# Kernel tuning notes

Hardware: AMD Instinct MI355X
Metric: run time of the kernel (lower is better)

## Reference

```python
import jax, jax.numpy as jnp
import numpy as np
import math

B, S, E = 16, 4096, 16      # batch, seq_len, n_experts
NE = 64                     # config.n_embd -> expert bottleneck dim
F = 4 * NE                  # n_state = 4*n_embd -> token feature dim


def gelu(x):
    # tanh-approx GELU exactly as in the source module
    c = math.sqrt(2.0 / math.pi)
    return 0.5 * x * (1.0 + jnp.tanh(c * (x + 0.044715 * x * x * x)))


def setup_inputs() -> dict:
    key = jax.random.key(0)
    ks = jax.random.split(key, 7)
    s1 = 1.0 / math.sqrt(F)   # fan-in init like nn.Linear(F, NE)
    s2 = 1.0 / math.sqrt(NE)  # fan-in init like nn.Linear(NE, F)
    return {
        "x":  jax.random.normal(ks[0], (B, S, F), jnp.float32),
        "W1": jax.random.uniform(ks[1], (E, F, NE), jnp.float32, -s1, s1),  # stacked c_fc
        "b1": jax.random.uniform(ks[2], (E, NE),    jnp.float32, -s1, s1),
        "W2": jax.random.uniform(ks[3], (E, NE, F), jnp.float32, -s2, s2),  # stacked c_proj
        "b2": jax.random.uniform(ks[4], (E, F),     jnp.float32, -s2, s2),
        "Wg": jax.random.uniform(ks[5], (F, E),     jnp.float32, -s1, s1),  # router
        "bg": jax.random.uniform(ks[6], (E,),       jnp.float32, -s1, s1),
    }


def reference(x, W1, b1, W2, b2, Wg, bg):
    # Router: per-token scores -> mean over sequence -> softmax over experts. [B, E]
    gate = jax.nn.softmax(jnp.mean(x @ Wg + bg, axis=1), axis=-1)
    # Dense all-experts FFN: [B, E, S, NE]
    h = gelu(jnp.einsum('bsf,efh->besh', x, W1) + b1[None, :, None, :])
    # [B, E, S, F]
    outs = jnp.einsum('besh,ehf->besf', h, W2) + b2[None, :, None, :]
    # Gate-weighted combine over experts -> [B, S, F]
    return jnp.einsum('be,besf->bsf', gate, outs)
```

## Files before the change

### kernel.cpp

```cpp
#include <hip/hip_runtime.h>
#include <hip/hip_bf16.h>
#include <stdint.h>

#define NB 16
#define NS 4096
#define NF 256
#define NH 64
#define NEXP 16

typedef __attribute__((ext_vector_type(8))) short     bf16x8;
typedef __attribute__((ext_vector_type(4))) float     f32x4;
typedef __attribute__((ext_vector_type(2))) unsigned  u32x2;
typedef __attribute__((ext_vector_type(8))) unsigned short u16x8;

#define PART_OFF   0u
#define GATE_OFF   524288u
#define BIASC_OFF  525312u
#define W1T_OFF    541696u
#define W2T_OFF    1065984u

__device__ __forceinline__ unsigned short bfr(float f) {
  unsigned u = __float_as_uint(f);
  u += 0x7fffu + ((u >> 16) & 1u);
  return (unsigned short)(u >> 16);
}
__device__ __forceinline__ unsigned pk(float a, float b) {
  __hip_bfloat162 t = __float22bfloat162_rn(make_float2(a, b));
  union { __hip_bfloat162 h; unsigned u; } cv; cv.h = t; return cv.u;
}
__device__ __forceinline__ bf16x8 as_bf(f32x4 v) {
  union { f32x4 f; bf16x8 h; } u; u.f = v; return u.h;
}
__device__ __forceinline__ void stage16(const void* g, void* l) {
  __builtin_amdgcn_global_load_lds((const __attribute__((address_space(1))) void*)g,
                                   (__attribute__((address_space(3))) void*)l, 16, 0, 0);
}

__global__ void k_pre(const float* __restrict__ x, const float* __restrict__ W1,
                      const float* __restrict__ W2, uint8_t* __restrict__ wsb) {
  const int blk = blockIdx.x;
  if (blk < 512) {
    const int b  = blk >> 5;
    const int ch = blk & 31;
    const int f  = threadIdx.x;
    const float* xp = x + ((size_t)b * NS + (size_t)ch * 128) * NF + f;
    float s = 0.0f;
    for (int i = 0; i < 128; ++i) s += xp[(size_t)i * NF];
    ((float*)(wsb + PART_OFF))[(size_t)(ch * 16 + b) * NF + f] = s;
    return;
  }
  const int u = (blk - 512) * 256 + threadIdx.x;
  u16x8 vals;
  if (u < 32768) {
    const int e  = u >> 11;
    const int r  = u & 2047;
    const int hd = r >> 5;
    const int kc = r & 31;
    const float* src = W1 + (size_t)e * (NF * NH) + (size_t)(kc * 8) * NH + hd;
#pragma unroll
    for (int j = 0; j < 8; ++j) vals[j] = bfr(src[(size_t)j * NH]);
    const int dst = (kc >> 2) * 4096 + hd * 64 + (kc & 3) * 16;
    *(u16x8*)(wsb + W1T_OFF + (size_t)e * 32768 + dst) = vals;
  } else {
    const int u2 = u - 32768;
    const int e  = u2 >> 11;
    const int r  = u2 & 2047;
    const int f  = r >> 3;
    const int hc = r & 7;
    const float* src = W2 + (size_t)e * (NH * NF) + (size_t)(hc * 8) * NF + f;
#pragma unroll
    for (int j = 0; j < 8; ++j) vals[j] = bfr(src[(size_t)j * NF]);
    const int dst = hc * 4096 + f * 16;
    *(u16x8*)(wsb + W2T_OFF + (size_t)e * 32768 + dst) = vals;
  }
}

__global__ void k_gate(const float* __restrict__ Wg, const float* __restrict__ bg,
                       const float* __restrict__ b2, uint8_t* __restrict__ wsb) {
  __shared__ float cs[16][256];
  __shared__ float lg[16][16];
  __shared__ float gs[16][16];
  const float* part  = (const float*)(wsb + PART_OFF);
  float* gate  = (float*)(wsb + GATE_OFF);
  float* biasc = (float*)(wsb + BIASC_OFF);
  const int t = threadIdx.x;
  for (int b = 0; b < 16; ++b) {
    float s = 0.0f;
    for (int ch = 0; ch < 32; ++ch) s += part[(size_t)(ch * 16 + b) * NF + t];
    cs[b][t] = s * (1.0f / 4096.0f);
  }
  __syncthreads();
  {
    const int b = t >> 4, e = t & 15;
    float acc = bg[e];
    for (int f = 0; f < NF; ++f) acc += cs[b][f] * Wg[f * 16 + e];
    lg[b][e] = acc;
  }
  __syncthreads();
  {
    const int b = t >> 4, e = t & 15;
    float m = lg[b][0];
    for (int j = 1; j < 16; ++j) m = fmaxf(m, lg[b][j]);
    float den = 0.0f;
    for (int j = 0; j < 16; ++j) den += __expf(lg[b][j] - m);
    float g = __expf(lg[b][e] - m) / den;
    gate[b * 16 + e] = g;
    gs[b][e] = g;
  }
  __syncthreads();
  for (int b = 0; b < 16; ++b) {
    float acc = 0.0f;
    for (int e = 0; e < 16; ++e) acc += gs[b][e] * b2[e * NF + t];
    biasc[b * NF + t] = acc;
  }
}

__global__ __launch_bounds__(768, 3)
void k_main(const float* __restrict__ x, const float* __restrict__ b1g,
            const uint8_t* __restrict__ wsb, float* __restrict__ out) {
  __shared__ __align__(16) uint8_t lds[98304];

  const int tid  = threadIdx.x;
  const int w    = tid >> 6;
  const int lane = tid & 63;
  const int c    = lane & 15;
  const int q    = lane >> 4;
  const bool g1  = (w < 4);
  const int fs   = (w - 4) * 32;
  const int st   = tid - 256;
  const int blk  = blockIdx.x;
  const int b    = blk >> 5;

  const float* gate_ws = (const float*)(wsb + GATE_OFF) + b * 16;
  const float* biasc   = (const float*)(wsb + BIASC_OFF) + b * NF;
  const uint8_t* w1src = wsb + W1T_OFF;
  const uint8_t* w2src = wsb + W2T_OFF;

  const f32x4 fz = {0.0f, 0.0f, 0.0f, 0.0f};
  f32x4 R[16];
  bf16x8 w2r[2][2];

  if (!g1) {
#pragma unroll
    for (int i = 0; i < 4; ++i)
      stage16(w1src + i * 8192 + st * 16, lds + i * 8192 + st * 16);
#pragma unroll
    for (int i = 0; i < 16; ++i) R[i] = fz;
  } else {
    const int row0 = blk * 128 + w * 32;
#pragma unroll
    for (int n = 0; n < 2; ++n) {
      const float* xp = x + (size_t)(row0 + n * 16 + c) * NF + q * 8;
#pragma unroll
      for (int ks = 0; ks < 8; ++ks) {
        f32x4 v0 = *(const f32x4*)(xp + ks * 32);
        f32x4 v1 = *(const f32x4*)(xp + ks * 32 + 4);
        union { unsigned u[4]; f32x4 f; } cv;
        cv.u[0] = pk(v0[0], v0[1]); cv.u[1] = pk(v0[2], v0[3]);
        cv.u[2] = pk(v1[0], v1[1]); cv.u[3] = pk(v1[2], v1[3]);
        R[n * 8 + ks] = cv.f;
      }
    }
  }

  __syncthreads();

  const float K1 = -2.3021858962f;
  const float KA = -0.102942243f;

#pragma unroll 1
  for (int e = 0; e < NEXP; ++e) {
    const int p  = e & 1;
    const int pn = p ^ 1;

    if (g1) {
      const uint8_t* w1p = lds + p * 32768;
      f32x4 a1[4][2];
#pragma unroll
      for (int m = 0; m < 4; ++m) { a1[m][0] = fz; a1[m][1] = fz; }
      __builtin_amdgcn_s_setprio(1);
#pragma unroll
      for (int ks = 0; ks < 8; ++ks) {
        bf16x8 am[4];
#pragma unroll
        for (int m = 0; m < 4; ++m)
          am[m] = *(const bf16x8*)(w1p + ks * 4096 + (m * 16 + c) * 64 + q * 16);
#pragma unroll
        for (int m = 0; m < 4; ++m) {
          a1[m][0] = __builtin_amdgcn_mfma_f32_16x16x32_bf16(am[m], as_bf(R[ks]),     a1[m][0], 0, 0, 0);
          a1[m][1] = __builtin_amdgcn_mfma_f32_16x16x32_bf16(am[m], as_bf(R[8 + ks]), a1[m][1], 0, 0, 0);
        }
      }
      __builtin_amdgcn_s_setprio(0);

      const float gv = gate_ws[e];
      uint8_t* htp = lds + 65536 + p * 16384;
#pragma unroll
      for (int m = 0; m < 4; ++m) {
        f32x4 b1v = *(const f32x4*)(b1g + e * NH + m * 16 + q * 4);
#pragma unroll
        for (int n = 0; n < 2; ++n) {
          f32x4 hv = a1[m][n] + b1v;
          float o[4];
#pragma unroll
          for (int r = 0; r < 4; ++r) {
            float xx = hv[r];
            float x2 = xx * xx;
            float tt = fmaf(KA, x2, K1);
            float ez = __builtin_amdgcn_exp2f(xx * tt);
            float rc = __builtin_amdgcn_rcpf(ez + 1.0f);
            o[r] = (gv * xx) * rc;
          }
          u32x2 hw;
          hw.x = pk(o[0], o[1]);
          hw.y = pk(o[2], o[3]);
          const int chunk = m * 2 + (q >> 1);
          const int tok   = w * 32 + n * 16 + c;
          *(u32x2*)(htp + chunk * 2048 + tok * 16 + (q & 1) * 8) = hw;
        }
      }
    } else {
      if (e < 15) {
        const uint8_t* src = w1src + (size_t)(e + 1) * 32768;
        uint8_t* dst = lds + pn * 32768;
#pragma unroll
        for (int i = 0; i < 4; ++i)
          stage16(src + i * 8192 + st * 16, dst + i * 8192 + st * 16);
      }

      if (e > 0) {
        const uint8_t* htp2 = lds + 65536 + pn * 16384;
        __builtin_amdgcn_s_setprio(1);
#pragma unroll
        for (int ks2 = 0; ks2 < 2; ++ks2) {
          bf16x8 bb2[8];
#pragma unroll
          for (int n2 = 0; n2 < 8; ++n2)
            bb2[n2] = *(const bf16x8*)(htp2 + (ks2 * 4 + q) * 2048 + (n2 * 16 + c) * 16);
#pragma unroll
          for (int m2 = 0; m2 < 2; ++m2)
#pragma unroll
            for (int n2 = 0; n2 < 8; ++n2)
              R[m2 * 8 + n2] = __builtin_amdgcn_mfma_f32_16x16x32_bf16(w2r[ks2][m2], bb2[n2], R[m2 * 8 + n2], 0, 0, 0);
        }
        __builtin_amdgcn_s_setprio(0);
      }

      const uint8_t* src = w2src + (size_t)e * 32768 + q * 4096 + (fs + c) * 16;
#pragma unroll
      for (int ks2 = 0; ks2 < 2; ++ks2)
#pragma unroll
        for (int m2 = 0; m2 < 2; ++m2)
          w2r[ks2][m2] = *(const bf16x8*)(src + ks2 * 16384 + m2 * 256);
    }

    __syncthreads();
  }

  if (!g1) {
    const uint8_t* htp2 = lds + 65536 + 16384;
#pragma unroll
    for (int ks2 = 0; ks2 < 2; ++ks2) {
      bf16x8 bb2[8];
#pragma unroll
      for (int n2 = 0; n2 < 8; ++n2)
        bb2[n2] = *(const bf16x8*)(htp2 + (ks2 * 4 + q) * 2048 + (n2 * 16 + c) * 16);
#pragma unroll
      for (int m2 = 0; m2 < 2; ++m2)
#pragma unroll
        for (int n2 = 0; n2 < 8; ++n2)
          R[m2 * 8 + n2] = __builtin_amdgcn_mfma_f32_16x16x32_bf16(w2r[ks2][m2], bb2[n2], R[m2 * 8 + n2], 0, 0, 0);
    }
#pragma unroll
    for (int m2 = 0; m2 < 2; ++m2) {
      const int fbase = fs + m2 * 16 + q * 4;
      f32x4 bc = *(const f32x4*)(biasc + fbase);
#pragma unroll
      for (int n2 = 0; n2 < 8; ++n2) {
        const int token = blk * 128 + n2 * 16 + c;
        f32x4 o = R[m2 * 8 + n2] + bc;
        *(f32x4*)(out + (size_t)token * NF + fbase) = o;
      }
    }
  }
}

extern "C" void kernel_launch(void* const* d_in, const int* in_sizes, int n_in,
                              void* d_out, int out_size, void* d_ws, size_t ws_size,
                              hipStream_t stream) {
  const float* x  = (const float*)d_in[0];
  const float* W1 = (const float*)d_in[1];
  const float* b1 = (const float*)d_in[2];
  const float* W2 = (const float*)d_in[3];
  const float* b2 = (const float*)d_in[4];
  const float* Wg = (const float*)d_in[5];
  const float* bg = (const float*)d_in[6];
  float* out = (float*)d_out;
  uint8_t* wsb = (uint8_t*)d_ws;

  k_pre<<<768, 256, 0, stream>>>(x, W1, W2, wsb);
  k_gate<<<1, 256, 0, stream>>>(Wg, bg, b2, wsb);
  k_main<<<512, 768, 0, stream>>>(x, b1, wsb, out);
}
```

Measured before the change: 124.1 us.

## Load W1 fragments directly from global into registers, shrink LDS to H buffers

Stops staging the per-expert W1 tile into LDS through the second warp group. The four GEMM1 waves now read their W1 fragments straight from global memory (L2) into registers, double-buffered one k-step ahead and prefetching the next expert's first step. LDS shrinks from 96KB to 32KB and holds only the double-buffered H tiles, which may let more blocks fit per CU. The full __syncthreads is replaced by an explicit lgkmcnt wait plus a raw barrier, so outstanding global loads no longer stall the barrier. The cost is global/L2 read traffic on the critical GEMM1 path and the latency of those loads.

```diff
diff --git a/kernel.cpp b/kernel.cpp
--- a/kernel.cpp
+++ b/kernel.cpp
@@ -30,10 +30,6 @@
 }
 __device__ __forceinline__ bf16x8 as_bf(f32x4 v) {
   union { f32x4 f; bf16x8 h; } u; u.f = v; return u.h;
-}
-__device__ __forceinline__ void stage16(const void* g, void* l) {
-  __builtin_amdgcn_global_load_lds((const __attribute__((address_space(1))) void*)g,
-                                   (__attribute__((address_space(3))) void*)l, 16, 0, 0);
 }
 
 __global__ void k_pre(const float* __restrict__ x, const float* __restrict__ W1,
@@ -118,7 +114,7 @@
 __global__ __launch_bounds__(768, 3)
 void k_main(const float* __restrict__ x, const float* __restrict__ b1g,
             const uint8_t* __restrict__ wsb, float* __restrict__ out) {
-  __shared__ __align__(16) uint8_t lds[98304];
+  __shared__ __align__(16) uint8_t lds[32768];
 
   const int tid  = threadIdx.x;
   const int w    = tid >> 6;
@@ -127,7 +123,6 @@
   const int q    = lane >> 4;
   const bool g1  = (w < 4);
   const int fs   = (w - 4) * 32;
-  const int st   = tid - 256;
   const int blk  = blockIdx.x;
   const int b    = blk >> 5;
 
@@ -139,11 +134,11 @@
   const f32x4 fz = {0.0f, 0.0f, 0.0f, 0.0f};
   f32x4 R[16];
   bf16x8 w2r[2][2];
+  bf16x8 am[2][4];
+
+  const uint8_t* w1lane = w1src + c * 64 + q * 16;
 
   if (!g1) {
-#pragma unroll
-    for (int i = 0; i < 4; ++i)
-      stage16(w1src + i * 8192 + st * 16, lds + i * 8192 + st * 16);
 #pragma unroll
     for (int i = 0; i < 16; ++i) R[i] = fz;
   } else {
@@ -161,9 +156,10 @@
         R[n * 8 + ks] = cv.f;
       }
     }
-  }
-
-  __syncthreads();
+#pragma unroll
+    for (int m = 0; m < 4; ++m)
+      am[0][m] = *(const bf16x8*)(w1lane + m * 1024);
+  }
 
   const float K1 = -2.3021858962f;
   const float KA = -0.102942243f;
@@ -174,27 +170,28 @@
     const int pn = p ^ 1;
 
     if (g1) {
-      const uint8_t* w1p = lds + p * 32768;
       f32x4 a1[4][2];
 #pragma unroll
       for (int m = 0; m < 4; ++m) { a1[m][0] = fz; a1[m][1] = fz; }
+      const uint8_t* w1e  = w1lane + (size_t)e * 32768;
+      const uint8_t* w1en = w1lane + (size_t)(e < 15 ? e + 1 : 15) * 32768;
       __builtin_amdgcn_s_setprio(1);
 #pragma unroll
       for (int ks = 0; ks < 8; ++ks) {
-        bf16x8 am[4];
+        const uint8_t* pf = (ks < 7) ? (w1e + (ks + 1) * 4096) : w1en;
 #pragma unroll
         for (int m = 0; m < 4; ++m)
-          am[m] = *(const bf16x8*)(w1p + ks * 4096 + (m * 16 + c) * 64 + q * 16);
+          am[(ks + 1) & 1][m] = *(const bf16x8*)(pf + m * 1024);
 #pragma unroll
         for (int m = 0; m < 4; ++m) {
-          a1[m][0] = __builtin_amdgcn_mfma_f32_16x16x32_bf16(am[m], as_bf(R[ks]),     a1[m][0], 0, 0, 0);
-          a1[m][1] = __builtin_amdgcn_mfma_f32_16x16x32_bf16(am[m], as_bf(R[8 + ks]), a1[m][1], 0, 0, 0);
+          a1[m][0] = __builtin_amdgcn_mfma_f32_16x16x32_bf16(am[ks & 1][m], as_bf(R[ks]),     a1[m][0], 0, 0, 0);
+          a1[m][1] = __builtin_amdgcn_mfma_f32_16x16x32_bf16(am[ks & 1][m], as_bf(R[8 + ks]), a1[m][1], 0, 0, 0);
         }
       }
       __builtin_amdgcn_s_setprio(0);
 
       const float gv = gate_ws[e];
-      uint8_t* htp = lds + 65536 + p * 16384;
+      uint8_t* htp = lds + p * 16384;
 #pragma unroll
       for (int m = 0; m < 4; ++m) {
         f32x4 b1v = *(const f32x4*)(b1g + e * NH + m * 16 + q * 4);
@@ -220,16 +217,8 @@
         }
       }
     } else {
-      if (e < 15) {
-        const uint8_t* src = w1src + (size_t)(e + 1) * 32768;
-        uint8_t* dst = lds + pn * 32768;
-#pragma unroll
-        for (int i = 0; i < 4; ++i)
-          stage16(src + i * 8192 + st * 16, dst + i * 8192 + st * 16);
-      }
-
       if (e > 0) {
-        const uint8_t* htp2 = lds + 65536 + pn * 16384;
+        const uint8_t* htp2 = lds + pn * 16384;
         __builtin_amdgcn_s_setprio(1);
 #pragma unroll
         for (int ks2 = 0; ks2 < 2; ++ks2) {
@@ -245,7 +234,6 @@
         }
         __builtin_amdgcn_s_setprio(0);
       }
-
       const uint8_t* src = w2src + (size_t)e * 32768 + q * 4096 + (fs + c) * 16;
 #pragma unroll
       for (int ks2 = 0; ks2 < 2; ++ks2)
@@ -254,11 +242,13 @@
           w2r[ks2][m2] = *(const bf16x8*)(src + ks2 * 16384 + m2 * 256);
     }
 
-    __syncthreads();
+    asm volatile("s_waitcnt lgkmcnt(0)" ::: "memory");
+    __builtin_amdgcn_s_barrier();
+    __builtin_amdgcn_sched_barrier(0);
   }
 
   if (!g1) {
-    const uint8_t* htp2 = lds + 65536 + 16384;
+    const uint8_t* htp2 = lds + 16384;
 #pragma unroll
     for (int ks2 = 0; ks2 < 2; ++ks2) {
       bf16x8 bb2[8];
```

After: 226.2 us. +82.2%, slower.

## Retile second GEMM per wave, double-buffer W1 LDS reads, split barriers

Applied to the files above, without the earlier changes.

Consumer waves now each own a 64-feature by 64-token tile of the W2 GEMM instead of 32 features by 128 tokens, which halves the per-wave LDS reads of hidden activations but doubles the W2 register fragments. The producer waves software-pipeline W1 fragment loads from LDS one k-step ahead, using two alternating register sets. The block-wide __syncthreads is replaced by role-specific waitcnt plus s_barrier, so consumer waves wait only on older global loads (vmcnt(8)) and the new W2 prefetch can stay in flight across the barrier. This relies on correct counter accounting, and the extra register pressure could hurt occupancy.

```diff
diff --git a/kernel.cpp b/kernel.cpp
--- a/kernel.cpp
+++ b/kernel.cpp
@@ -126,7 +126,8 @@
   const int c    = lane & 15;
   const int q    = lane >> 4;
   const bool g1  = (w < 4);
-  const int fs   = (w - 4) * 32;
+  const int fs   = ((w - 4) >> 1) * 64;
+  const int ts   = ((w - 4) & 1) * 64;
   const int st   = tid - 256;
   const int blk  = blockIdx.x;
   const int b    = blk >> 5;
@@ -138,7 +139,7 @@
 
   const f32x4 fz = {0.0f, 0.0f, 0.0f, 0.0f};
   f32x4 R[16];
-  bf16x8 w2r[2][2];
+  bf16x8 w2r[2][4];
 
   if (!g1) {
 #pragma unroll
@@ -175,20 +176,33 @@
 
     if (g1) {
       const uint8_t* w1p = lds + p * 32768;
+      bf16x8 am0[4], am1[4];
+#pragma unroll
+      for (int m = 0; m < 4; ++m)
+        am0[m] = *(const bf16x8*)(w1p + (m * 16 + c) * 64 + q * 16);
       f32x4 a1[4][2];
 #pragma unroll
       for (int m = 0; m < 4; ++m) { a1[m][0] = fz; a1[m][1] = fz; }
       __builtin_amdgcn_s_setprio(1);
 #pragma unroll
       for (int ks = 0; ks < 8; ++ks) {
-        bf16x8 am[4];
-#pragma unroll
-        for (int m = 0; m < 4; ++m)
-          am[m] = *(const bf16x8*)(w1p + ks * 4096 + (m * 16 + c) * 64 + q * 16);
+        if (ks < 7) {
+          const uint8_t* nxt = w1p + (ks + 1) * 4096;
+          if (ks & 1) {
+#pragma unroll
+            for (int m = 0; m < 4; ++m)
+              am0[m] = *(const bf16x8*)(nxt + (m * 16 + c) * 64 + q * 16);
+          } else {
+#pragma unroll
+            for (int m = 0; m < 4; ++m)
+              am1[m] = *(const bf16x8*)(nxt + (m * 16 + c) * 64 + q * 16);
+          }
+        }
 #pragma unroll
         for (int m = 0; m < 4; ++m) {
-          a1[m][0] = __builtin_amdgcn_mfma_f32_16x16x32_bf16(am[m], as_bf(R[ks]),     a1[m][0], 0, 0, 0);
-          a1[m][1] = __builtin_amdgcn_mfma_f32_16x16x32_bf16(am[m], as_bf(R[8 + ks]), a1[m][1], 0, 0, 0);
+          bf16x8 a = (ks & 1) ? am1[m] : am0[m];
+          a1[m][0] = __builtin_amdgcn_mfma_f32_16x16x32_bf16(a, as_bf(R[ks]),     a1[m][0], 0, 0, 0);
+          a1[m][1] = __builtin_amdgcn_mfma_f32_16x16x32_bf16(a, as_bf(R[8 + ks]), a1[m][1], 0, 0, 0);
         }
       }
       __builtin_amdgcn_s_setprio(0);
@@ -219,6 +233,9 @@
           *(u32x2*)(htp + chunk * 2048 + tok * 16 + (q & 1) * 8) = hw;
         }
       }
+      asm volatile("s_waitcnt lgkmcnt(0)" ::: "memory");
+      __builtin_amdgcn_s_barrier();
+      __builtin_amdgcn_sched_barrier(0);
     } else {
       if (e < 15) {
         const uint8_t* src = w1src + (size_t)(e + 1) * 32768;
@@ -227,58 +244,65 @@
         for (int i = 0; i < 4; ++i)
           stage16(src + i * 8192 + st * 16, dst + i * 8192 + st * 16);
       }
+      __builtin_amdgcn_sched_barrier(0);
 
       if (e > 0) {
         const uint8_t* htp2 = lds + 65536 + pn * 16384;
+        bf16x8 bb[2][4];
+#pragma unroll
+        for (int ks2 = 0; ks2 < 2; ++ks2)
+#pragma unroll
+          for (int n2 = 0; n2 < 4; ++n2)
+            bb[ks2][n2] = *(const bf16x8*)(htp2 + (ks2 * 4 + q) * 2048 + (ts + n2 * 16 + c) * 16);
         __builtin_amdgcn_s_setprio(1);
 #pragma unroll
-        for (int ks2 = 0; ks2 < 2; ++ks2) {
-          bf16x8 bb2[8];
-#pragma unroll
-          for (int n2 = 0; n2 < 8; ++n2)
-            bb2[n2] = *(const bf16x8*)(htp2 + (ks2 * 4 + q) * 2048 + (n2 * 16 + c) * 16);
-#pragma unroll
-          for (int m2 = 0; m2 < 2; ++m2)
-#pragma unroll
-            for (int n2 = 0; n2 < 8; ++n2)
-              R[m2 * 8 + n2] = __builtin_amdgcn_mfma_f32_16x16x32_bf16(w2r[ks2][m2], bb2[n2], R[m2 * 8 + n2], 0, 0, 0);
-        }
+        for (int ks2 = 0; ks2 < 2; ++ks2)
+#pragma unroll
+          for (int m2 = 0; m2 < 4; ++m2)
+#pragma unroll
+            for (int n2 = 0; n2 < 4; ++n2)
+              R[m2 * 4 + n2] = __builtin_amdgcn_mfma_f32_16x16x32_bf16(w2r[ks2][m2], bb[ks2][n2], R[m2 * 4 + n2], 0, 0, 0);
         __builtin_amdgcn_s_setprio(0);
       }
 
-      const uint8_t* src = w2src + (size_t)e * 32768 + q * 4096 + (fs + c) * 16;
-#pragma unroll
-      for (int ks2 = 0; ks2 < 2; ++ks2)
-#pragma unroll
-        for (int m2 = 0; m2 < 2; ++m2)
-          w2r[ks2][m2] = *(const bf16x8*)(src + ks2 * 16384 + m2 * 256);
+      {
+        const uint8_t* src = w2src + (size_t)e * 32768 + q * 4096 + (fs + c) * 16;
+#pragma unroll
+        for (int ks2 = 0; ks2 < 2; ++ks2)
+#pragma unroll
+          for (int m2 = 0; m2 < 4; ++m2)
+            w2r[ks2][m2] = *(const bf16x8*)(src + ks2 * 16384 + m2 * 256);
+      }
+
+      asm volatile("s_waitcnt vmcnt(8) lgkmcnt(0)" ::: "memory");
+      __builtin_amdgcn_s_barrier();
+      __builtin_amdgcn_sched_barrier(0);
     }
-
-    __syncthreads();
   }
 
   if (!g1) {
     const uint8_t* htp2 = lds + 65536 + 16384;
-#pragma unroll
-    for (int ks2 = 0; ks2 < 2; ++ks2) {
-      bf16x8 bb2[8];
-#pragma unroll
-      for (int n2 = 0; n2 < 8; ++n2)
-        bb2[n2] = *(const bf16x8*)(htp2 + (ks2 * 4 + q) * 2048 + (n2 * 16 + c) * 16);
-#pragma unroll
-      for (int m2 = 0; m2 < 2; ++m2)
-#pragma unroll
-        for (int n2 = 0; n2 < 8; ++n2)
-          R[m2 * 8 + n2] = __builtin_amdgcn_mfma_f32_16x16x32_bf16(w2r[ks2][m2], bb2[n2], R[m2 * 8 + n2], 0, 0, 0);
-    }
-#pragma unroll
-    for (int m2 = 0; m2 < 2; ++m2) {
+    bf16x8 bb[2][4];
+#pragma unroll
+    for (int ks2 = 0; ks2 < 2; ++ks2)
+#pragma unroll
+      for (int n2 = 0; n2 < 4; ++n2)
+        bb[ks2][n2] = *(const bf16x8*)(htp2 + (ks2 * 4 + q) * 2048 + (ts + n2 * 16 + c) * 16);
+#pragma unroll
+    for (int ks2 = 0; ks2 < 2; ++ks2)
+#pragma unroll
+      for (int m2 = 0; m2 < 4; ++m2)
+#pragma unroll
+        for (int n2 = 0; n2 < 4; ++n2)
+          R[m2 * 4 + n2] = __builtin_amdgcn_mfma_f32_16x16x32_bf16(w2r[ks2][m2], bb[ks2][n2], R[m2 * 4 + n2], 0, 0, 0);
+#pragma unroll
+    for (int m2 = 0; m2 < 4; ++m2) {
       const int fbase = fs + m2 * 16 + q * 4;
       f32x4 bc = *(const f32x4*)(biasc + fbase);
 #pragma unroll
-      for (int n2 = 0; n2 < 8; ++n2) {
-        const int token = blk * 128 + n2 * 16 + c;
-        f32x4 o = R[m2 * 8 + n2] + bc;
+      for (int n2 = 0; n2 < 4; ++n2) {
+        const int token = blk * 128 + ts + n2 * 16 + c;
+        f32x4 o = R[m2 * 4 + n2] + bc;
         *(f32x4*)(out + (size_t)token * NF + fbase) = o;
       }
     }
```

Result: slower. 144.2 us (+16.2%).

## Split fused MoE kernel into separate hidden-activation and output kernels via workspace

Applied to the files above, without the earlier changes.

Replaces the warp-specialized fused kernel with two kernels when the workspace is large enough. The first computes GELU hidden activations for all experts and writes them to global memory as bf16. The second reads them back, scales W2 by the gate in registers, and accumulates the output with a larger per-wave tile and register double-buffering. This removes the producer/consumer LDS handoff and per-expert barriers, at the cost of writing and re-reading a 128 MB intermediate and one extra launch. The fused kernel is kept as a fallback.

```diff
diff --git a/kernel.cpp b/kernel.cpp
--- a/kernel.cpp
+++ b/kernel.cpp
@@ -18,6 +18,8 @@
 #define BIASC_OFF  525312u
 #define W1T_OFF    541696u
 #define W2T_OFF    1065984u
+#define H_OFF      1590272u
+#define WS_NEED    (1590272ull + 134217728ull)
 
 __device__ __forceinline__ unsigned short bfr(float f) {
   unsigned u = __float_as_uint(f);
@@ -115,11 +117,203 @@
   }
 }
 
+__global__ __launch_bounds__(256, 2)
+void k_h(const float* __restrict__ x, const float* __restrict__ b1g,
+         const uint8_t* __restrict__ wsb, uint8_t* __restrict__ hbuf) {
+  __shared__ __align__(16) uint8_t lds[65536];
+
+  const int tid  = threadIdx.x;
+  const int w    = tid >> 6;
+  const int lane = tid & 63;
+  const int c    = lane & 15;
+  const int q    = lane >> 4;
+  const int blk  = blockIdx.x;
+  const int gtok0 = blk * 128 + w * 32;
+  const uint8_t* w1src = wsb + W1T_OFF;
+
+#pragma unroll
+  for (int i = 0; i < 8; ++i)
+    stage16(w1src + i * 4096 + tid * 16, lds + i * 4096 + tid * 16);
+
+  bf16x8 xf[16];
+#pragma unroll
+  for (int n = 0; n < 2; ++n) {
+    const float* xp = x + (size_t)(gtok0 + n * 16 + c) * NF + q * 8;
+#pragma unroll
+    for (int ks = 0; ks < 8; ++ks) {
+      f32x4 v0 = *(const f32x4*)(xp + ks * 32);
+      f32x4 v1 = *(const f32x4*)(xp + ks * 32 + 4);
+      union { unsigned u[4]; bf16x8 h; } cv;
+      cv.u[0] = pk(v0[0], v0[1]); cv.u[1] = pk(v0[2], v0[3]);
+      cv.u[2] = pk(v1[0], v1[1]); cv.u[3] = pk(v1[2], v1[3]);
+      xf[n * 8 + ks] = cv.h;
+    }
+  }
+
+  __syncthreads();
+
+  const float K1 = -2.3021858962f;
+  const float KA = -0.102942243f;
+  const f32x4 fz = {0.0f, 0.0f, 0.0f, 0.0f};
+
+#pragma unroll 1
+  for (int e = 0; e < NEXP; ++e) {
+    const int p = e & 1;
+    if (e < 15) {
+      const uint8_t* src = w1src + (size_t)(e + 1) * 32768;
+      uint8_t* dst = lds + (p ^ 1) * 32768;
+#pragma unroll
+      for (int i = 0; i < 8; ++i)
+        stage16(src + i * 4096 + tid * 16, dst + i * 4096 + tid * 16);
+    }
+
+    const uint8_t* w1p = lds + p * 32768;
+    f32x4 a1[4][2];
+#pragma unroll
+    for (int m = 0; m < 4; ++m) { a1[m][0] = fz; a1[m][1] = fz; }
+    __builtin_amdgcn_s_setprio(1);
+#pragma unroll
+    for (int ks = 0; ks < 8; ++ks) {
+      bf16x8 am[4];
+#pragma unroll
+      for (int m = 0; m < 4; ++m)
+        am[m] = *(const bf16x8*)(w1p + ks * 4096 + (m * 16 + c) * 64 + q * 16);
+#pragma unroll
+      for (int m = 0; m < 4; ++m) {
+        a1[m][0] = __builtin_amdgcn_mfma_f32_16x16x32_bf16(am[m], xf[ks],     a1[m][0], 0, 0, 0);
+        a1[m][1] = __builtin_amdgcn_mfma_f32_16x16x32_bf16(am[m], xf[8 + ks], a1[m][1], 0, 0, 0);
+      }
+    }
+    __builtin_amdgcn_s_setprio(0);
+
+    uint8_t* he = hbuf + (size_t)e * 8388608;
+#pragma unroll
+    for (int m = 0; m < 4; ++m) {
+      f32x4 b1v = *(const f32x4*)(b1g + e * NH + m * 16 + q * 4);
+#pragma unroll
+      for (int n = 0; n < 2; ++n) {
+        f32x4 hv = a1[m][n] + b1v;
+        float o[4];
+#pragma unroll
+        for (int r = 0; r < 4; ++r) {
+          float xx = hv[r];
+          float tt = fmaf(KA, xx * xx, K1);
+          float ez = __builtin_amdgcn_exp2f(xx * tt);
+          o[r] = xx * __builtin_amdgcn_rcpf(ez + 1.0f);
+        }
+        u32x2 hw;
+        hw.x = pk(o[0], o[1]);
+        hw.y = pk(o[2], o[3]);
+        *(u32x2*)(he + (size_t)(gtok0 + n * 16 + c) * 128 + m * 32 + q * 8) = hw;
+      }
+    }
+
+    __syncthreads();
+  }
+}
+
+__device__ __forceinline__ void ko_loadh(bf16x8 (&h)[8], const uint8_t* hbuf, int e,
+                                         int gtok0, int c, int q) {
+  const uint8_t* src = hbuf + (size_t)e * 8388608 + (size_t)(gtok0 + c) * 128 + q * 16;
+#pragma unroll
+  for (int n2 = 0; n2 < 4; ++n2)
+#pragma unroll
+    for (int ks2 = 0; ks2 < 2; ++ks2)
+      h[n2 * 2 + ks2] = *(const bf16x8*)(src + n2 * 2048 + ks2 * 64);
+}
+__device__ __forceinline__ void ko_loadw(f32x4 (&wr)[8], const uint8_t* w2src, int e,
+                                         int fs, int c, int q) {
+  const uint8_t* src = w2src + (size_t)e * 32768 + q * 4096 + (fs + c) * 16;
+#pragma unroll
+  for (int ks2 = 0; ks2 < 2; ++ks2)
+#pragma unroll
+    for (int m2 = 0; m2 < 4; ++m2)
+      wr[ks2 * 4 + m2] = *(const f32x4*)(src + ks2 * 16384 + m2 * 256);
+}
+__device__ __forceinline__ void ko_mma(f32x4 (&acc)[16], const f32x4 (&wr)[8],
+                                       const bf16x8 (&h)[8], float g) {
+  bf16x8 ws[8];
+#pragma unroll
+  for (int i = 0; i < 8; ++i) {
+    union { f32x4 f; unsigned u[4]; } in; in.f = wr[i];
+    union { unsigned u[4]; bf16x8 h; } o;
+#pragma unroll
+    for (int j = 0; j < 4; ++j) {
+      float lo = __uint_as_float(in.u[j] << 16) * g;
+      float hi = __uint_as_float(in.u[j] & 0xffff0000u) * g;
+      o.u[j] = pk(lo, hi);
+    }
+    ws[i] = o.h;
+  }
+  __builtin_amdgcn_s_setprio(1);
+#pragma unroll
+  for (int ks2 = 0; ks2 < 2; ++ks2)
+#pragma unroll
+    for (int m2 = 0; m2 < 4; ++m2)
+#pragma unroll
+      for (int n2 = 0; n2 < 4; ++n2)
+        acc[m2 * 4 + n2] = __builtin_amdgcn_mfma_f32_16x16x32_bf16(ws[ks2 * 4 + m2], h[n2 * 2 + ks2], acc[m2 * 4 + n2], 0, 0, 0);
+  __builtin_amdgcn_s_setprio(0);
+}
+
+__global__ __launch_bounds__(256, 2)
+void k_o(const uint8_t* __restrict__ wsb, const uint8_t* __restrict__ hbuf,
+         float* __restrict__ out) {
+  const int tid  = threadIdx.x;
+  const int w    = tid >> 6;
+  const int lane = tid & 63;
+  const int c    = lane & 15;
+  const int q    = lane >> 4;
+  const int blk  = blockIdx.x;
+  const int gtok0 = blk * 64;
+  const int b    = blk >> 6;
+  const int fs   = w * 64;
+
+  const float* gate_ws = (const float*)(wsb + GATE_OFF) + b * 16;
+  const float* biasc   = (const float*)(wsb + BIASC_OFF) + b * NF;
+  const uint8_t* w2src = wsb + W2T_OFF;
+
+  const f32x4 fz = {0.0f, 0.0f, 0.0f, 0.0f};
+  f32x4 acc[16];
+#pragma unroll
+  for (int i = 0; i < 16; ++i) acc[i] = fz;
+
+  bf16x8 hA[8], hB[8];
+  f32x4  wA[8], wB[8];
+
+  ko_loadh(hA, hbuf, 0, gtok0, c, q);
+  ko_loadw(wA, w2src, 0, fs, c, q);
+
+#pragma unroll 1
+  for (int eb = 0; eb < 8; ++eb) {
+    const int e0 = 2 * eb;
+    ko_loadh(hB, hbuf, e0 + 1, gtok0, c, q);
+    ko_loadw(wB, w2src, e0 + 1, fs, c, q);
+    ko_mma(acc, wA, hA, gate_ws[e0]);
+    if (e0 + 2 < 16) {
+      ko_loadh(hA, hbuf, e0 + 2, gtok0, c, q);
+      ko_loadw(wA, w2src, e0 + 2, fs, c, q);
+    }
+    ko_mma(acc, wB, hB, gate_ws[e0 + 1]);
+  }
+
+#pragma unroll
+  for (int m2 = 0; m2 < 4; ++m2) {
+    const int fbase = fs + m2 * 16 + q * 4;
+    f32x4 bc = *(const f32x4*)(biasc + fbase);
+#pragma unroll
+    for (int n2 = 0; n2 < 4; ++n2) {
+      const int token = gtok0 + n2 * 16 + c;
+      f32x4 o = acc[m2 * 4 + n2] + bc;
+      *(f32x4*)(out + (size_t)token * NF + fbase) = o;
+    }
+  }
+}
+
 __global__ __launch_bounds__(768, 3)
-void k_main(const float* __restrict__ x, const float* __restrict__ b1g,
-            const uint8_t* __restrict__ wsb, float* __restrict__ out) {
+void k_main_fused(const float* __restrict__ x, const float* __restrict__ b1g,
+                  const uint8_t* __restrict__ wsb, float* __restrict__ out) {
   __shared__ __align__(16) uint8_t lds[98304];
-
   const int tid  = threadIdx.x;
   const int w    = tid >> 6;
   const int lane = tid & 63;
@@ -130,16 +324,13 @@
   const int st   = tid - 256;
   const int blk  = blockIdx.x;
   const int b    = blk >> 5;
-
   const float* gate_ws = (const float*)(wsb + GATE_OFF) + b * 16;
   const float* biasc   = (const float*)(wsb + BIASC_OFF) + b * NF;
   const uint8_t* w1src = wsb + W1T_OFF;
   const uint8_t* w2src = wsb + W2T_OFF;
-
   const f32x4 fz = {0.0f, 0.0f, 0.0f, 0.0f};
   f32x4 R[16];
   bf16x8 w2r[2][2];
-
   if (!g1) {
 #pragma unroll
     for (int i = 0; i < 4; ++i)
@@ -162,17 +353,13 @@
       }
     }
   }
-
   __syncthreads();
-
   const float K1 = -2.3021858962f;
   const float KA = -0.102942243f;
-
 #pragma unroll 1
   for (int e = 0; e < NEXP; ++e) {
     const int p  = e & 1;
     const int pn = p ^ 1;
-
     if (g1) {
       const uint8_t* w1p = lds + p * 32768;
       f32x4 a1[4][2];
@@ -192,7 +379,6 @@
         }
       }
       __builtin_amdgcn_s_setprio(0);
-
       const float gv = gate_ws[e];
       uint8_t* htp = lds + 65536 + p * 16384;
 #pragma unroll
@@ -205,11 +391,9 @@
 #pragma unroll
           for (int r = 0; r < 4; ++r) {
             float xx = hv[r];
-            float x2 = xx * xx;
-            float tt = fmaf(KA, x2, K1);
+            float tt = fmaf(KA, xx * xx, K1);
             float ez = __builtin_amdgcn_exp2f(xx * tt);
-            float rc = __builtin_amdgcn_rcpf(ez + 1.0f);
-            o[r] = (gv * xx) * rc;
+            o[r] = (gv * xx) * __builtin_amdgcn_rcpf(ez + 1.0f);
           }
           u32x2 hw;
           hw.x = pk(o[0], o[1]);
@@ -227,7 +411,6 @@
         for (int i = 0; i < 4; ++i)
           stage16(src + i * 8192 + st * 16, dst + i * 8192 + st * 16);
       }
-
       if (e > 0) {
         const uint8_t* htp2 = lds + 65536 + pn * 16384;
         __builtin_amdgcn_s_setprio(1);
@@ -245,7 +428,6 @@
         }
         __builtin_amdgcn_s_setprio(0);
       }
-
       const uint8_t* src = w2src + (size_t)e * 32768 + q * 4096 + (fs + c) * 16;
 #pragma unroll
       for (int ks2 = 0; ks2 < 2; ++ks2)
@@ -253,10 +435,8 @@
         for (int m2 = 0; m2 < 2; ++m2)
           w2r[ks2][m2] = *(const bf16x8*)(src + ks2 * 16384 + m2 * 256);
     }
-
     __syncthreads();
   }
-
   if (!g1) {
     const uint8_t* htp2 = lds + 65536 + 16384;
 #pragma unroll
@@ -300,5 +480,11 @@
 
   k_pre<<<768, 256, 0, stream>>>(x, W1, W2, wsb);
   k_gate<<<1, 256, 0, stream>>>(Wg, bg, b2, wsb);
-  k_main<<<512, 768, 0, stream>>>(x, b1, wsb, out);
-}
+  if (ws_size >= WS_NEED) {
+    uint8_t* hbuf = wsb + H_OFF;
+    k_h<<<512, 256, 0, stream>>>(x, b1, wsb, hbuf);
+    k_o<<<1024, 256, 0, stream>>>(wsb, hbuf, out);
+  } else {
+    k_main_fused<<<512, 768, 0, stream>>>(x, b1, wsb, out);
+  }
+}
```

Result: slower. 183.1 us (+47.6%).
